# Kernel optimization log

Hardware: AMD Instinct MI355X
Metric: run time of the kernel (lower is better)

The kernel has to match this reference:

```python
import jax, jax.numpy as jnp
import numpy as np

BS = 64
N_TGT = 5000


def setup_inputs() -> dict:
    key = jax.random.key(0)
    k0, k1, k2, kb, kr = jax.random.split(key, 5)
    pred0 = jax.random.normal(k0, (BS, 11, 160, 160), dtype=jnp.float32)
    pred1 = jax.random.normal(k1, (BS, 11, 80, 80), dtype=jnp.float32)
    pred2 = jax.random.normal(k2, (BS, 11, 40, 40), dtype=jnp.float32)
    # targets: [batch_idx, x_frac, y_frac, w, h, cls] per row
    bidx = jax.random.randint(kb, (N_TGT, 1), 0, BS).astype(jnp.float32)
    rest = jax.random.uniform(kr, (N_TGT, 5), dtype=jnp.float32)
    targets = jnp.concatenate([bidx, rest], axis=1)
    return {"pred0": pred0, "pred1": pred1, "pred2": pred2, "targets": targets}


def _bce_mean(p, t):
    # matches torch F.binary_cross_entropy: logs clamped at -100
    logp = jnp.maximum(jnp.log(p), -100.0)
    log1mp = jnp.maximum(jnp.log1p(-p), -100.0)
    return jnp.mean(-(t * logp + (1.0 - t) * log1mp))


def _obj_loss(pred, targets):
    bs, _, h, w = pred.shape
    obj_pred = jax.nn.sigmoid(pred[:, 4:5, :, :])  # [bs,1,h,w]
    b = targets[:, 0]
    gx = (targets[:, 1] * w).astype(jnp.int32)  # trunc like int()
    gy = (targets[:, 2] * h).astype(jnp.int32)
    valid = (b < bs) & (gx >= 0) & (gx < w) & (gy >= 0) & (gy < h)
    # route invalid rows to an out-of-range batch index; mode='drop' discards them
    bi = jnp.where(valid, b.astype(jnp.int32), bs)
    obj_target = jnp.zeros_like(obj_pred).at[bi, 0, gy, gx].set(1.0, mode="drop")
    return _bce_mean(obj_pred, obj_target)


def reference(pred0, pred1, pred2, targets):
    loss_obj = (_obj_loss(pred0, targets)
                + _obj_loss(pred1, targets)
                + _obj_loss(pred2, targets))
    # loss_box and loss_cls are identically zero in the source module
    return loss_obj * 1.0
```

## Files before the change

kernel.cpp:

```cpp
#include <hip/hip_runtime.h>
#include <math.h>

constexpr int BS_   = 64;
constexpr int NTGT  = 5000;
constexpr int H0 = 160, H1 = 80, H2 = 40;
constexpr int HW0 = H0 * H0;
constexpr int HW1 = H1 * H1;
constexpr int HW2 = H2 * H2;
constexpr int N0 = BS_ * HW0;
constexpr int N1 = BS_ * HW1;
constexpr int N2 = BS_ * HW2;
constexpr int Q0 = N0 / 4, Q1 = N1 / 4, Q2 = N2 / 4;
constexpr int QTOT = Q0 + Q1 + Q2;
constexpr int GRID = 2048;
constexpr int TPB  = 256;
constexpr int TBL  = 4096;
constexpr int NPART = 16;
constexpr int NCORR = 3 * NPART;

__device__ __forceinline__ float sp_clamp(float x) {
    float u = expf(-fabsf(x));
    return fminf(fmaxf(x, 0.0f) + logf(1.0f + u), 100.0f);
}

__global__ __launch_bounds__(TPB) void fused_kernel(
        const float* __restrict__ p0, const float* __restrict__ p1,
        const float* __restrict__ p2, const float* __restrict__ tgt,
        float* __restrict__ ws) {
    __shared__ unsigned tbl[TBL];
    __shared__ float red[TPB / 64];

    float acc = 0.0f;

    const int stride = GRID * TPB;
    for (int idx = blockIdx.x * TPB + threadIdx.x; idx < QTOT; idx += stride) {
        const float* base;
        int qhw, q;
        float w;
        if (idx < Q0)            { base = p0; qhw = HW0 / 4; q = idx;           w = 1.0f / N0; }
        else if (idx < Q0 + Q1)  { base = p1; qhw = HW1 / 4; q = idx - Q0;      w = 1.0f / N1; }
        else                     { base = p2; qhw = HW2 / 4; q = idx - Q0 - Q1; w = 1.0f / N2; }
        int b   = q / qhw;
        int rem = q - b * qhw;
        const float4 x4 = *reinterpret_cast<const float4*>(
            base + (size_t)(b * 11 + 4) * (size_t)(qhw * 4) + (size_t)rem * 4);
        acc += (sp_clamp(x4.x) + sp_clamp(x4.y) + sp_clamp(x4.z) + sp_clamp(x4.w)) * w;
    }

    if (blockIdx.x < NCORR) {
        const int level      = blockIdx.x >> 4;
        const unsigned part  = blockIdx.x & (NPART - 1);
        for (int i = threadIdx.x; i < TBL; i += TPB) tbl[i] = 0xFFFFFFFFu;
        __syncthreads();

        const float* base;
        int h;
        float wgt;
        if (level == 0)      { base = p0; h = H0; wgt = 1.0f / N0; }
        else if (level == 1) { base = p1; h = H1; wgt = 1.0f / N1; }
        else                 { base = p2; h = H2; wgt = 1.0f / N2; }

        for (int t = threadIdx.x; t < NTGT; t += TPB) {
            float bf = tgt[t * 6 + 0];
            float tx = tgt[t * 6 + 1];
            float ty = tgt[t * 6 + 2];
            int gx = (int)(tx * (float)h);
            int gy = (int)(ty * (float)h);
            if (!(bf < (float)BS_ && gx >= 0 && gx < h && gy >= 0 && gy < h)) continue;
            int b = (int)bf;
            if (b < 0) continue;

            unsigned cell = (unsigned)((b * h + gy) * h + gx);
            if ((cell & (NPART - 1)) != part) continue;

            unsigned slot = (cell * 2654435761u) >> 20;
            bool isNew = false;
            for (int pr = 0; pr < TBL; ++pr) {
                unsigned prev = atomicCAS(&tbl[slot], 0xFFFFFFFFu, cell);
                if (prev == 0xFFFFFFFFu) { isNew = true; break; }
                if (prev == cell) break;
                slot = (slot + 1) & (TBL - 1);
            }
            if (isNew) {
                float x = base[(size_t)(b * 11 + 4) * (size_t)(h * h) + gy * h + gx];
                acc += (sp_clamp(-x) - sp_clamp(x)) * wgt;
            }
        }
    }

    #pragma unroll
    for (int off = 32; off > 0; off >>= 1) acc += __shfl_down(acc, off, 64);
    const int lane = threadIdx.x & 63;
    const int wid  = threadIdx.x >> 6;
    if (lane == 0) red[wid] = acc;
    __syncthreads();
    if (threadIdx.x == 0)
        ws[blockIdx.x] = red[0] + red[1] + red[2] + red[3];
}

__global__ __launch_bounds__(TPB) void final_reduce(const float* __restrict__ ws,
                                                    float* __restrict__ out) {
    __shared__ float red[TPB / 64];
    float acc = 0.0f;
    #pragma unroll
    for (int i = threadIdx.x; i < GRID; i += TPB) acc += ws[i];
    #pragma unroll
    for (int off = 32; off > 0; off >>= 1) acc += __shfl_down(acc, off, 64);
    const int lane = threadIdx.x & 63;
    const int wid  = threadIdx.x >> 6;
    if (lane == 0) red[wid] = acc;
    __syncthreads();
    if (threadIdx.x == 0)
        out[0] = red[0] + red[1] + red[2] + red[3];
}

extern "C" void kernel_launch(void* const* d_in, const int* in_sizes, int n_in,
                              void* d_out, int out_size, void* d_ws, size_t ws_size,
                              hipStream_t stream) {
    const float* p0  = (const float*)d_in[0];
    const float* p1  = (const float*)d_in[1];
    const float* p2  = (const float*)d_in[2];
    const float* tgt = (const float*)d_in[3];
    float* out = (float*)d_out;
    float* ws  = (float*)d_ws;

    fused_kernel<<<GRID, TPB, 0, stream>>>(p0, p1, p2, tgt, ws);
    final_reduce<<<1, TPB, 0, stream>>>(ws, out);
}
```

Baseline: 23.71 us.

## Split correction blocks from base blocks, templatize level indexing, use fast exp/log

```diff
diff --git a/kernel.cpp b/kernel.cpp
--- a/kernel.cpp
+++ b/kernel.cpp
@@ -17,10 +17,20 @@
 constexpr int TBL  = 4096;
 constexpr int NPART = 16;
 constexpr int NCORR = 3 * NPART;
+constexpr int NBASE = GRID - NCORR;
 
 __device__ __forceinline__ float sp_clamp(float x) {
-    float u = expf(-fabsf(x));
-    return fminf(fmaxf(x, 0.0f) + logf(1.0f + u), 100.0f);
+    float u = __expf(-fabsf(x));
+    return fminf(fmaxf(x, 0.0f) + __logf(1.0f + u), 100.0f);
+}
+
+template <int HWQ>
+__device__ __forceinline__ float base_elem(const float* __restrict__ base, int q) {
+    int b   = q / HWQ;
+    int rem = q - b * HWQ;
+    const float4 x4 = *reinterpret_cast<const float4*>(
+        base + (size_t)(b * 11 + 4) * (size_t)(HWQ * 4) + (size_t)rem * 4);
+    return sp_clamp(x4.x) + sp_clamp(x4.y) + sp_clamp(x4.z) + sp_clamp(x4.w);
 }
 
 __global__ __launch_bounds__(TPB) void fused_kernel(
@@ -32,22 +42,17 @@
 
     float acc = 0.0f;
 
-    const int stride = GRID * TPB;
-    for (int idx = blockIdx.x * TPB + threadIdx.x; idx < QTOT; idx += stride) {
-        const float* base;
-        int qhw, q;
-        float w;
-        if (idx < Q0)            { base = p0; qhw = HW0 / 4; q = idx;           w = 1.0f / N0; }
-        else if (idx < Q0 + Q1)  { base = p1; qhw = HW1 / 4; q = idx - Q0;      w = 1.0f / N1; }
-        else                     { base = p2; qhw = HW2 / 4; q = idx - Q0 - Q1; w = 1.0f / N2; }
-        int b   = q / qhw;
-        int rem = q - b * qhw;
-        const float4 x4 = *reinterpret_cast<const float4*>(
-            base + (size_t)(b * 11 + 4) * (size_t)(qhw * 4) + (size_t)rem * 4);
-        acc += (sp_clamp(x4.x) + sp_clamp(x4.y) + sp_clamp(x4.z) + sp_clamp(x4.w)) * w;
-    }
-
-    if (blockIdx.x < NCORR) {
+    if (blockIdx.x >= NCORR) {
+        const int stride = NBASE * TPB;
+        for (int idx = (blockIdx.x - NCORR) * TPB + threadIdx.x; idx < QTOT; idx += stride) {
+            if (idx < Q0)
+                acc += base_elem<HW0 / 4>(p0, idx) * (1.0f / N0);
+            else if (idx < Q0 + Q1)
+                acc += base_elem<HW1 / 4>(p1, idx - Q0) * (1.0f / N1);
+            else
+                acc += base_elem<HW2 / 4>(p2, idx - Q0 - Q1) * (1.0f / N2);
+        }
+    } else {
         const int level      = blockIdx.x >> 4;
         const unsigned part  = blockIdx.x & (NPART - 1);
         for (int i = threadIdx.x; i < TBL; i += TPB) tbl[i] = 0xFFFFFFFFu;
@@ -60,30 +65,34 @@
         else if (level == 1) { base = p1; h = H1; wgt = 1.0f / N1; }
         else                 { base = p2; h = H2; wgt = 1.0f / N2; }
 
-        for (int t = threadIdx.x; t < NTGT; t += TPB) {
-            float bf = tgt[t * 6 + 0];
-            float tx = tgt[t * 6 + 1];
-            float ty = tgt[t * 6 + 2];
-            int gx = (int)(tx * (float)h);
-            int gy = (int)(ty * (float)h);
-            if (!(bf < (float)BS_ && gx >= 0 && gx < h && gy >= 0 && gy < h)) continue;
-            int b = (int)bf;
-            if (b < 0) continue;
-
-            unsigned cell = (unsigned)((b * h + gy) * h + gx);
-            if ((cell & (NPART - 1)) != part) continue;
-
-            unsigned slot = (cell * 2654435761u) >> 20;
-            bool isNew = false;
-            for (int pr = 0; pr < TBL; ++pr) {
-                unsigned prev = atomicCAS(&tbl[slot], 0xFFFFFFFFu, cell);
-                if (prev == 0xFFFFFFFFu) { isNew = true; break; }
-                if (prev == cell) break;
-                slot = (slot + 1) & (TBL - 1);
-            }
-            if (isNew) {
-                float x = base[(size_t)(b * 11 + 4) * (size_t)(h * h) + gy * h + gx];
-                acc += (sp_clamp(-x) - sp_clamp(x)) * wgt;
+        #pragma unroll 4
+        for (int t0 = 0; t0 < NTGT; t0 += TPB) {
+            const int t = t0 + (int)threadIdx.x;
+            if (t < NTGT) {
+                const float2 bt = *reinterpret_cast<const float2*>(tgt + (size_t)t * 6);
+                const float  ty = tgt[(size_t)t * 6 + 2];
+                int gx = (int)(bt.y * (float)h);
+                int gy = (int)(ty   * (float)h);
+                if (bt.x < (float)BS_ && gx >= 0 && gx < h && gy >= 0 && gy < h) {
+                    int b = (int)bt.x;
+                    if (b >= 0) {
+                        unsigned cell = (unsigned)((b * h + gy) * h + gx);
+                        if ((cell & (NPART - 1)) == part) {
+                            unsigned slot = (cell * 2654435761u) >> 20;
+                            bool isNew = false;
+                            for (int pr = 0; pr < TBL; ++pr) {
+                                unsigned prev = atomicCAS(&tbl[slot], 0xFFFFFFFFu, cell);
+                                if (prev == 0xFFFFFFFFu) { isNew = true; break; }
+                                if (prev == cell) break;
+                                slot = (slot + 1) & (TBL - 1);
+                            }
+                            if (isNew) {
+                                float x = base[(size_t)(b * 11 + 4) * (size_t)(h * h) + gy * h + gx];
+                                acc += (sp_clamp(-x) - sp_clamp(x)) * wgt;
+                            }
+                        }
+                    }
+                }
             }
         }
     }
```

Result: faster. 20.37 us (-14.1%).
